# Kernel optimization log

Hardware: AMD Instinct MI355X
Metric: run time of the kernel (lower is better)

## Reference

```python
import jax, jax.numpy as jnp
import numpy as np

N_ATOMS = 500_000
N_PAIRS = 16_000_000
A0 = 0.5291772105638411
KE = 14.399645351950548
KEHALF = KE / 2.0


def softplus_inverse(x):
    # inverse of softplus: log(exp(x) - 1)
    return float(np.log(np.expm1(x)))


def setup_inputs() -> dict:
    key = jax.random.key(0)
    k_z, k_r, k_c, k_i, k_j = jax.random.split(key, 5)
    Zf = jax.random.randint(k_z, (N_ATOMS,), 1, 95).astype(jnp.float32)
    rij = jax.random.uniform(k_r, (N_PAIRS,), minval=0.5, maxval=5.0, dtype=jnp.float32)
    cutoff_values = jax.random.uniform(k_c, (N_PAIRS,), dtype=jnp.float32)
    idx_i = jax.random.randint(k_i, (N_PAIRS,), 0, N_ATOMS)
    idx_j = jax.random.randint(k_j, (N_PAIRS,), 0, N_ATOMS)
    p = lambda v: jnp.full((1,), softplus_inverse(v), dtype=jnp.float32)
    return {
        "N": N_ATOMS,
        "Zf": Zf,
        "rij": rij,
        "cutoff_values": cutoff_values,
        "idx_i": idx_i,
        "idx_j": idx_j,
        "adiv": p(1.0 / (0.8854 * A0)),
        "apow": p(0.23),
        "c1": p(0.1818),
        "c2": p(0.5099),
        "c3": p(0.2802),
        "c4": p(0.02817),
        "a1": p(3.2),
        "a2": p(0.9423),
        "a3": p(0.4028),
        "a4": p(0.2016),
    }


def reference(N, Zf, rij, cutoff_values, idx_i, idx_j,
              adiv, apow, c1, c2, c3, c4, a1, a2, a3, a4):
    sp = jax.nn.softplus
    # per-atom screened charge: [N]
    z = Zf ** sp(apow)
    # per-pair screening length: [P]
    a = (z[idx_i] + z[idx_j]) * sp(adiv)
    a1p = sp(a1) * a
    a2p = sp(a2) * a
    a3p = sp(a3) * a
    a4p = sp(a4) * a
    c1p, c2p, c3p, c4p = sp(c1), sp(c2), sp(c3), sp(c4)
    csum = c1p + c2p + c3p + c4p
    c1n, c2n, c3n, c4n = c1p / csum, c2p / csum, c3p / csum, c4p / csum
    zizj = Zf[idx_i] * Zf[idx_j]
    f = (c1n * jnp.exp(-a1p * rij)
         + c2n * jnp.exp(-a2p * rij)
         + c3n * jnp.exp(-a3p * rij)
         + c4n * jnp.exp(-a4p * rij)) * cutoff_values
    contrib = KEHALF * f * zizj / rij  # [P]
    return jnp.zeros((N,), dtype=Zf.dtype).at[idx_i].add(contrib)
```

## Files before the change

kernel.cpp:

```cpp
#include <hip/hip_runtime.h>
#include <hip/hip_fp16.h>

static constexpr float KEHALF = 7.199822675975274f;
static constexpr int APB = 2048;
static constexpr int APB_SHIFT = 11;
static constexpr int NBMAX = 256;
static constexpr int CHUNK = 8192;
static constexpr int ABLK = 512;
static constexpr int BBLK = 1024;
static constexpr int CTILE = 2048;

typedef float v4f __attribute__((ext_vector_type(4)));
typedef int   v4i __attribute__((ext_vector_type(4)));
typedef unsigned v4u __attribute__((ext_vector_type(4)));

__global__ void zbl_tables_kernel(const float* __restrict__ adiv,
                                  const float* __restrict__ apow,
                                  const float* __restrict__ c1,
                                  const float* __restrict__ c2,
                                  const float* __restrict__ c3,
                                  const float* __restrict__ c4,
                                  const float* __restrict__ a1,
                                  const float* __restrict__ a2,
                                  const float* __restrict__ a3,
                                  const float* __restrict__ a4,
                                  float* __restrict__ consts,
                                  float* __restrict__ lutA) {
    __shared__ float sA[2];
    int t = threadIdx.x;
    if (t == 0) {
        auto sp = [](float x) { return log1pf(expf(x)); };
        float c1p = sp(*c1), c2p = sp(*c2), c3p = sp(*c3), c4p = sp(*c4);
        float inv = 1.0f / (c1p + c2p + c3p + c4p);
        consts[0] = sp(*apow);
        consts[1] = sp(*adiv);
        consts[2] = c1p * inv; consts[3] = c2p * inv;
        consts[4] = c3p * inv; consts[5] = c4p * inv;
        consts[6] = sp(*a1); consts[7] = sp(*a2);
        consts[8] = sp(*a3); consts[9] = sp(*a4);
        sA[0] = consts[0]; sA[1] = consts[1];
    }
    __syncthreads();
    if (t < 96)
        lutA[t] = (t == 0) ? 0.0f : sA[1] * expf(sA[0] * logf((float)t));
}

__global__ void zbl_pack_kernel(const float* __restrict__ Zf,
                                unsigned char* __restrict__ zb, int N) {
    int i = blockIdx.x * blockDim.x + threadIdx.x;
    if (i < N) zb[i] = (unsigned char)(Zf[i] + 0.5f);
}

__global__ void __launch_bounds__(ABLK)
zbl_phaseA(const int* __restrict__ idx_i, const int* __restrict__ idx_j,
           const float* __restrict__ rij, const float* __restrict__ cut,
           const unsigned char* __restrict__ zb,
           const float* __restrict__ consts, const float* __restrict__ lutA,
           unsigned* __restrict__ recs, unsigned short* __restrict__ starts,
           int P, int NB) {
    __shared__ unsigned hist[NBMAX];
    __shared__ unsigned scanv[NBMAX];
    __shared__ unsigned cursor[NBMAX];
    __shared__ float lA[96];
    __shared__ unsigned stage[CHUNK];

    const int t = threadIdx.x;
    const int c = blockIdx.x;
    const int base = c * CHUNK;
    const int lim = min(base + CHUNK, P);
    const int cnt = lim - base;
    const int n4 = cnt >> 2;

    for (int b = t; b < NBMAX; b += ABLK) hist[b] = 0;
    if (t < 96) lA[t] = lutA[t];
    __syncthreads();

    {
        const v4i* ii4 = reinterpret_cast<const v4i*>(idx_i + base);
        for (int q = t; q < n4; q += ABLK) {
            v4i ii = __builtin_nontemporal_load(ii4 + q);
            atomicAdd(&hist[(unsigned)ii[0] >> APB_SHIFT], 1u);
            atomicAdd(&hist[(unsigned)ii[1] >> APB_SHIFT], 1u);
            atomicAdd(&hist[(unsigned)ii[2] >> APB_SHIFT], 1u);
            atomicAdd(&hist[(unsigned)ii[3] >> APB_SHIFT], 1u);
        }
        for (int p = n4 * 4 + t; p < cnt; p += ABLK)
            atomicAdd(&hist[(unsigned)idx_i[base + p] >> APB_SHIFT], 1u);
    }
    __syncthreads();

    if (t < NBMAX) scanv[t] = hist[t];
    __syncthreads();
    for (int off = 1; off < NBMAX; off <<= 1) {
        unsigned v = 0;
        if (t < NBMAX && t >= off) v = scanv[t - off];
        __syncthreads();
        if (t < NBMAX && t >= off) scanv[t] += v;
        __syncthreads();
    }
    if (t < NBMAX) cursor[t] = scanv[t] - hist[t];
    {
        const int S = NB + 1;
        for (int b = t; b <= NB; b += ABLK)
            starts[(size_t)c * S + b] =
                (unsigned short)(b == 0 ? 0u : scanv[b - 1]);
    }
    __syncthreads();

    const float c1n = consts[2], c2n = consts[3], c3n = consts[4], c4n = consts[5];
    const float a1 = consts[6], a2 = consts[7], a3 = consts[8], a4 = consts[9];

    auto process = [&](int i, int j, float r, float cu) {
        unsigned bi = zb[i], bj = zb[j];
        float aij = lA[bi] + lA[bj];
        float ar = aij * r;
        float f = c1n * __expf(-a1 * ar) + c2n * __expf(-a2 * ar)
                + c3n * __expf(-a3 * ar) + c4n * __expf(-a4 * ar);
        float contrib = KEHALF * f * cu * (float)bi * (float)bj *
                        __builtin_amdgcn_rcpf(r);
        unsigned b = (unsigned)i >> APB_SHIFT;
        unsigned rank = atomicAdd(&cursor[b], 1u);
        stage[rank] = (((unsigned)i & (APB - 1)) << 16)
                    | (unsigned)__half_as_ushort(__float2half_rn(contrib));
    };

    {
        const v4i* ii4 = reinterpret_cast<const v4i*>(idx_i + base);
        const v4i* jj4 = reinterpret_cast<const v4i*>(idx_j + base);
        const v4f* rr4 = reinterpret_cast<const v4f*>(rij + base);
        const v4f* cc4 = reinterpret_cast<const v4f*>(cut + base);
        for (int q = t; q < n4; q += ABLK) {
            v4i ii = __builtin_nontemporal_load(ii4 + q);
            v4i jj = __builtin_nontemporal_load(jj4 + q);
            v4f rr = __builtin_nontemporal_load(rr4 + q);
            v4f cc = __builtin_nontemporal_load(cc4 + q);
#pragma unroll
            for (int k = 0; k < 4; ++k) process(ii[k], jj[k], rr[k], cc[k]);
        }
        for (int p = n4 * 4 + t; p < cnt; p += ABLK)
            process(idx_i[base + p], idx_j[base + p], rij[base + p], cut[base + p]);
    }
    __syncthreads();

    {
        const v4u* src = reinterpret_cast<const v4u*>(stage);
        v4u* dst = reinterpret_cast<v4u*>(recs + (size_t)base);
        for (int k = t; k < CHUNK / 4; k += ABLK)
            __builtin_nontemporal_store(src[k], dst + k);
    }
}

__global__ void __launch_bounds__(BBLK)
zbl_phaseB(const unsigned* __restrict__ recs,
           const unsigned short* __restrict__ starts,
           float* __restrict__ out, int N, int NB, int nchunks) {
    __shared__ float acc[APB];
    __shared__ unsigned short s0s[CTILE];
    __shared__ unsigned short s1s[CTILE];
    const int t = threadIdx.x;
    const int b = blockIdx.x;
    const int S = NB + 1;
    for (int i = t; i < APB; i += BBLK) acc[i] = 0.f;

    const int wave = t >> 6, lane = t & 63, nw = BBLK / 64;

    for (int cb = 0; cb < nchunks; cb += CTILE) {
        const int ce = min(cb + CTILE, nchunks);
        __syncthreads();
        for (int c = cb + t; c < ce; c += BBLK) {
            s0s[c - cb] = starts[(size_t)c * S + b];
            s1s[c - cb] = starts[(size_t)c * S + b + 1];
        }
        __syncthreads();
        for (int c = cb + wave; c < ce; c += nw) {
            unsigned s0 = s0s[c - cb], s1 = s1s[c - cb];
            const unsigned* seg = recs + (size_t)c * CHUNK;
            for (unsigned u = s0 + lane; u < s1; u += 64) {
                unsigned rec = __builtin_nontemporal_load(seg + u);
                float v = __half2float(__ushort_as_half((unsigned short)(rec & 0xffffu)));
                atomicAdd(&acc[rec >> 16], v);
            }
        }
    }
    __syncthreads();

    const int abase = b << APB_SHIFT;
    for (int i = t; i < APB; i += BBLK) {
        int g = abase + i;
        if (g < N) out[g] = acc[i];
    }
}

__global__ void __launch_bounds__(256)
zbl_pair_fallback(const v4f* __restrict__ rij4, const v4f* __restrict__ cut4,
                  const v4i* __restrict__ ii4, const v4i* __restrict__ jj4,
                  const float* __restrict__ Zf, const float* __restrict__ consts,
                  float* __restrict__ out, int P4) {
    int t = blockIdx.x * blockDim.x + threadIdx.x;
    if (t >= P4) return;
    const float sp_apow = consts[0], sp_adiv = consts[1];
    const float c1n = consts[2], c2n = consts[3], c3n = consts[4], c4n = consts[5];
    const float a1 = consts[6], a2 = consts[7], a3 = consts[8], a4 = consts[9];
    v4f rr = rij4[t]; v4f cc = cut4[t]; v4i ii = ii4[t]; v4i jj = jj4[t];
#pragma unroll
    for (int k = 0; k < 4; ++k) {
        int i = ii[k], j = jj[k];
        float zfi = Zf[i], zfj = Zf[j];
        float zi = __expf(sp_apow * __logf(zfi));
        float zj = __expf(sp_apow * __logf(zfj));
        float a = (zi + zj) * sp_adiv;
        float ar = a * rr[k];
        float f = c1n * __expf(-a1 * ar) + c2n * __expf(-a2 * ar)
                + c3n * __expf(-a3 * ar) + c4n * __expf(-a4 * ar);
        atomicAdd(&out[i],
                  KEHALF * f * cc[k] * zfi * zfj * __builtin_amdgcn_rcpf(rr[k]));
    }
}

extern "C" void kernel_launch(void* const* d_in, const int* in_sizes, int n_in,
                              void* d_out, int out_size, void* d_ws, size_t ws_size,
                              hipStream_t stream) {
    const float* Zf = (const float*)d_in[1];
    const float* rij = (const float*)d_in[2];
    const float* cut = (const float*)d_in[3];
    const int* idx_i = (const int*)d_in[4];
    const int* idx_j = (const int*)d_in[5];
    const int N = in_sizes[1];
    const int P = in_sizes[2];
    float* out = (float*)d_out;

    const int NB = (N + APB - 1) / APB;
    const int nchunks = (P + CHUNK - 1) / CHUNK;

    size_t recs_bytes = (size_t)nchunks * CHUNK * 4;
    size_t starts_bytes = (size_t)nchunks * (NB + 1) * 2;
    size_t consts_off = (recs_bytes + starts_bytes + 255) & ~(size_t)255;
    size_t lut_off = consts_off + 16 * 4;
    size_t zb_off = lut_off + 96 * 4;
    size_t need = zb_off + (size_t)N + 64;

    if (NB <= NBMAX && ws_size >= need) {
        unsigned* recs = (unsigned*)d_ws;
        unsigned short* starts = (unsigned short*)((char*)d_ws + recs_bytes);
        float* consts = (float*)((char*)d_ws + consts_off);
        float* lutA = (float*)((char*)d_ws + lut_off);
        unsigned char* zb = (unsigned char*)((char*)d_ws + zb_off);

        zbl_tables_kernel<<<1, 128, 0, stream>>>(
            (const float*)d_in[6], (const float*)d_in[7],
            (const float*)d_in[8], (const float*)d_in[9],
            (const float*)d_in[10], (const float*)d_in[11],
            (const float*)d_in[12], (const float*)d_in[13],
            (const float*)d_in[14], (const float*)d_in[15], consts, lutA);

        zbl_pack_kernel<<<(N + 255) / 256, 256, 0, stream>>>(Zf, zb, N);

        zbl_phaseA<<<nchunks, ABLK, 0, stream>>>(
            idx_i, idx_j, rij, cut, zb, consts, lutA, recs, starts, P, NB);

        zbl_phaseB<<<NB, BBLK, 0, stream>>>(recs, starts, out, N, NB, nchunks);
    } else {
        float* consts = (float*)d_ws;
        float* lutA = consts + 16;
        hipMemsetAsync(out, 0, (size_t)out_size * sizeof(float), stream);
        zbl_tables_kernel<<<1, 128, 0, stream>>>(
            (const float*)d_in[6], (const float*)d_in[7],
            (const float*)d_in[8], (const float*)d_in[9],
            (const float*)d_in[10], (const float*)d_in[11],
            (const float*)d_in[12], (const float*)d_in[13],
            (const float*)d_in[14], (const float*)d_in[15], consts, lutA);
        zbl_pair_fallback<<<(P / 4 + 255) / 256, 256, 0, stream>>>(
            (const v4f*)rij, (const v4f*)cut, (const v4i*)idx_i,
            (const v4i*)idx_j, Zf, consts, out, P / 4);
    }
}
```

Before: 488.2 us.

## Split phase B over chunk ranges and drop phase A LDS staging

Phase B now runs on a 2D grid that splits the chunk range across up to 16 blocks per atom bucket. Each block atomically adds its partial sums into a zeroed output, and each 32-lane half-wave walks one segment. Phase A drops the LDS staging buffer and the per-element LUT, scattering records straight to global memory and computing z^p with exp/log inline. It also replaces the block-wide barrier scan with a wave-shuffle scan and keeps the loaded idx_i vectors in registers for reuse. The intent is more parallelism and occupancy in phase B and fewer barriers and less LDS in phase A, at the cost of uncoalesced global stores, extra transcendental math, and global float atomics.

```diff
diff --git a/kernel.cpp b/kernel.cpp
--- a/kernel.cpp
+++ b/kernel.cpp
@@ -8,7 +8,8 @@
 static constexpr int CHUNK = 8192;
 static constexpr int ABLK = 512;
 static constexpr int BBLK = 1024;
-static constexpr int CTILE = 2048;
+static constexpr int CTILE = 1024;
+static constexpr int NW_SCAN = NBMAX / 64;
 
 typedef float v4f __attribute__((ext_vector_type(4)));
 typedef int   v4i __attribute__((ext_vector_type(4)));
@@ -24,11 +25,8 @@
                                   const float* __restrict__ a2,
                                   const float* __restrict__ a3,
                                   const float* __restrict__ a4,
-                                  float* __restrict__ consts,
-                                  float* __restrict__ lutA) {
-    __shared__ float sA[2];
-    int t = threadIdx.x;
-    if (t == 0) {
+                                  float* __restrict__ consts) {
+    if (threadIdx.x == 0) {
         auto sp = [](float x) { return log1pf(expf(x)); };
         float c1p = sp(*c1), c2p = sp(*c2), c3p = sp(*c3), c4p = sp(*c4);
         float inv = 1.0f / (c1p + c2p + c3p + c4p);
@@ -38,11 +36,7 @@
         consts[4] = c3p * inv; consts[5] = c4p * inv;
         consts[6] = sp(*a1); consts[7] = sp(*a2);
         consts[8] = sp(*a3); consts[9] = sp(*a4);
-        sA[0] = consts[0]; sA[1] = consts[1];
-    }
-    __syncthreads();
-    if (t < 96)
-        lutA[t] = (t == 0) ? 0.0f : sA[1] * expf(sA[0] * logf((float)t));
+    }
 }
 
 __global__ void zbl_pack_kernel(const float* __restrict__ Zf,
@@ -55,14 +49,12 @@
 zbl_phaseA(const int* __restrict__ idx_i, const int* __restrict__ idx_j,
            const float* __restrict__ rij, const float* __restrict__ cut,
            const unsigned char* __restrict__ zb,
-           const float* __restrict__ consts, const float* __restrict__ lutA,
+           const float* __restrict__ consts,
            unsigned* __restrict__ recs, unsigned short* __restrict__ starts,
            int P, int NB) {
     __shared__ unsigned hist[NBMAX];
-    __shared__ unsigned scanv[NBMAX];
     __shared__ unsigned cursor[NBMAX];
-    __shared__ float lA[96];
-    __shared__ unsigned stage[CHUNK];
+    __shared__ unsigned wsum[NW_SCAN];
 
     const int t = threadIdx.x;
     const int c = blockIdx.x;
@@ -72,110 +64,122 @@
     const int n4 = cnt >> 2;
 
     for (int b = t; b < NBMAX; b += ABLK) hist[b] = 0;
-    if (t < 96) lA[t] = lutA[t];
-    __syncthreads();
-
-    {
-        const v4i* ii4 = reinterpret_cast<const v4i*>(idx_i + base);
-        for (int q = t; q < n4; q += ABLK) {
-            v4i ii = __builtin_nontemporal_load(ii4 + q);
-            atomicAdd(&hist[(unsigned)ii[0] >> APB_SHIFT], 1u);
-            atomicAdd(&hist[(unsigned)ii[1] >> APB_SHIFT], 1u);
-            atomicAdd(&hist[(unsigned)ii[2] >> APB_SHIFT], 1u);
-            atomicAdd(&hist[(unsigned)ii[3] >> APB_SHIFT], 1u);
-        }
-        for (int p = n4 * 4 + t; p < cnt; p += ABLK)
-            atomicAdd(&hist[(unsigned)idx_i[base + p] >> APB_SHIFT], 1u);
-    }
-    __syncthreads();
-
-    if (t < NBMAX) scanv[t] = hist[t];
-    __syncthreads();
-    for (int off = 1; off < NBMAX; off <<= 1) {
-        unsigned v = 0;
-        if (t < NBMAX && t >= off) v = scanv[t - off];
-        __syncthreads();
-        if (t < NBMAX && t >= off) scanv[t] += v;
-        __syncthreads();
-    }
-    if (t < NBMAX) cursor[t] = scanv[t] - hist[t];
-    {
-        const int S = NB + 1;
-        for (int b = t; b <= NB; b += ABLK)
-            starts[(size_t)c * S + b] =
-                (unsigned short)(b == 0 ? 0u : scanv[b - 1]);
-    }
-    __syncthreads();
-
+    __syncthreads();
+
+    const v4i* ii4 = reinterpret_cast<const v4i*>(idx_i + base);
+    const bool p0 = t < n4;
+    const bool p1 = ABLK + t < n4;
+    const bool p2 = 2 * ABLK + t < n4;
+    const bool p3 = 3 * ABLK + t < n4;
+    v4i ii0{}, ii1{}, ii2{}, ii3{};
+    if (p0) ii0 = __builtin_nontemporal_load(ii4 + t);
+    if (p1) ii1 = __builtin_nontemporal_load(ii4 + ABLK + t);
+    if (p2) ii2 = __builtin_nontemporal_load(ii4 + 2 * ABLK + t);
+    if (p3) ii3 = __builtin_nontemporal_load(ii4 + 3 * ABLK + t);
+
+    auto hist4 = [&](v4i ii) {
+        atomicAdd(&hist[(unsigned)ii[0] >> APB_SHIFT], 1u);
+        atomicAdd(&hist[(unsigned)ii[1] >> APB_SHIFT], 1u);
+        atomicAdd(&hist[(unsigned)ii[2] >> APB_SHIFT], 1u);
+        atomicAdd(&hist[(unsigned)ii[3] >> APB_SHIFT], 1u);
+    };
+    if (p0) hist4(ii0);
+    if (p1) hist4(ii1);
+    if (p2) hist4(ii2);
+    if (p3) hist4(ii3);
+    for (int p = n4 * 4 + t; p < cnt; p += ABLK)
+        atomicAdd(&hist[(unsigned)idx_i[base + p] >> APB_SHIFT], 1u);
+    __syncthreads();
+
+    unsigned hv = (t < NBMAX) ? hist[t] : 0u;
+    unsigned v = hv;
+#pragma unroll
+    for (int off = 1; off < 64; off <<= 1) {
+        unsigned n = __shfl_up(v, off, 64);
+        if ((t & 63) >= off) v += n;
+    }
+    if (t < NBMAX && (t & 63) == 63) wsum[t >> 6] = v;
+    __syncthreads();
+    const int S = NB + 1;
+    if (t < NBMAX) {
+        unsigned pre = 0;
+#pragma unroll
+        for (int w = 0; w < NW_SCAN - 1; ++w)
+            if (w < (t >> 6)) pre += wsum[w];
+        unsigned inc = v + pre;
+        cursor[t] = inc - hv;
+        if (t < NB)
+            starts[(size_t)c * S + t + 1] = (unsigned short)inc;
+    }
+    if (t == 0) starts[(size_t)c * S] = 0;
+    __syncthreads();
+
+    const float sp_apow = consts[0], sp_adiv = consts[1];
     const float c1n = consts[2], c2n = consts[3], c3n = consts[4], c4n = consts[5];
     const float a1 = consts[6], a2 = consts[7], a3 = consts[8], a4 = consts[9];
 
     auto process = [&](int i, int j, float r, float cu) {
         unsigned bi = zb[i], bj = zb[j];
-        float aij = lA[bi] + lA[bj];
-        float ar = aij * r;
+        float fi = (float)bi, fj = (float)bj;
+        float zi = __expf(sp_apow * __logf(fi));
+        float zj = __expf(sp_apow * __logf(fj));
+        float ar = (zi + zj) * sp_adiv * r;
         float f = c1n * __expf(-a1 * ar) + c2n * __expf(-a2 * ar)
                 + c3n * __expf(-a3 * ar) + c4n * __expf(-a4 * ar);
-        float contrib = KEHALF * f * cu * (float)bi * (float)bj *
-                        __builtin_amdgcn_rcpf(r);
+        float contrib = KEHALF * f * cu * fi * fj * __builtin_amdgcn_rcpf(r);
         unsigned b = (unsigned)i >> APB_SHIFT;
         unsigned rank = atomicAdd(&cursor[b], 1u);
-        stage[rank] = (((unsigned)i & (APB - 1)) << 16)
-                    | (unsigned)__half_as_ushort(__float2half_rn(contrib));
+        unsigned rec = (((unsigned)i & (APB - 1)) << 16)
+                     | (unsigned)__half_as_ushort(__float2half_rn(contrib));
+        recs[(size_t)base + rank] = rec;
     };
 
-    {
-        const v4i* ii4 = reinterpret_cast<const v4i*>(idx_i + base);
-        const v4i* jj4 = reinterpret_cast<const v4i*>(idx_j + base);
-        const v4f* rr4 = reinterpret_cast<const v4f*>(rij + base);
-        const v4f* cc4 = reinterpret_cast<const v4f*>(cut + base);
-        for (int q = t; q < n4; q += ABLK) {
-            v4i ii = __builtin_nontemporal_load(ii4 + q);
-            v4i jj = __builtin_nontemporal_load(jj4 + q);
-            v4f rr = __builtin_nontemporal_load(rr4 + q);
-            v4f cc = __builtin_nontemporal_load(cc4 + q);
-#pragma unroll
-            for (int k = 0; k < 4; ++k) process(ii[k], jj[k], rr[k], cc[k]);
-        }
-        for (int p = n4 * 4 + t; p < cnt; p += ABLK)
-            process(idx_i[base + p], idx_j[base + p], rij[base + p], cut[base + p]);
-    }
-    __syncthreads();
-
-    {
-        const v4u* src = reinterpret_cast<const v4u*>(stage);
-        v4u* dst = reinterpret_cast<v4u*>(recs + (size_t)base);
-        for (int k = t; k < CHUNK / 4; k += ABLK)
-            __builtin_nontemporal_store(src[k], dst + k);
-    }
+    const v4i* jj4 = reinterpret_cast<const v4i*>(idx_j + base);
+    const v4f* rr4 = reinterpret_cast<const v4f*>(rij + base);
+    const v4f* cc4 = reinterpret_cast<const v4f*>(cut + base);
+    auto group = [&](v4i ii, int q) {
+        v4i jj = __builtin_nontemporal_load(jj4 + q);
+        v4f rr = __builtin_nontemporal_load(rr4 + q);
+        v4f cc = __builtin_nontemporal_load(cc4 + q);
+#pragma unroll
+        for (int k = 0; k < 4; ++k) process(ii[k], jj[k], rr[k], cc[k]);
+    };
+    if (p0) group(ii0, t);
+    if (p1) group(ii1, ABLK + t);
+    if (p2) group(ii2, 2 * ABLK + t);
+    if (p3) group(ii3, 3 * ABLK + t);
+    for (int p = n4 * 4 + t; p < cnt; p += ABLK)
+        process(idx_i[base + p], idx_j[base + p], rij[base + p], cut[base + p]);
 }
 
 __global__ void __launch_bounds__(BBLK)
 zbl_phaseB(const unsigned* __restrict__ recs,
            const unsigned short* __restrict__ starts,
-           float* __restrict__ out, int N, int NB, int nchunks) {
+           float* __restrict__ out, int N, int NB, int nchunks, int cpb) {
     __shared__ float acc[APB];
     __shared__ unsigned short s0s[CTILE];
     __shared__ unsigned short s1s[CTILE];
     const int t = threadIdx.x;
     const int b = blockIdx.x;
+    const int c0 = blockIdx.y * cpb;
+    const int c1e = min(c0 + cpb, nchunks);
     const int S = NB + 1;
     for (int i = t; i < APB; i += BBLK) acc[i] = 0.f;
 
-    const int wave = t >> 6, lane = t & 63, nw = BBLK / 64;
-
-    for (int cb = 0; cb < nchunks; cb += CTILE) {
-        const int ce = min(cb + CTILE, nchunks);
+    const int hw = t >> 5, hl = t & 31, nhw = BBLK / 32;
+
+    for (int cb = c0; cb < c1e; cb += CTILE) {
+        const int ce = min(cb + CTILE, c1e);
         __syncthreads();
         for (int c = cb + t; c < ce; c += BBLK) {
             s0s[c - cb] = starts[(size_t)c * S + b];
             s1s[c - cb] = starts[(size_t)c * S + b + 1];
         }
         __syncthreads();
-        for (int c = cb + wave; c < ce; c += nw) {
+        for (int c = cb + hw; c < ce; c += nhw) {
             unsigned s0 = s0s[c - cb], s1 = s1s[c - cb];
             const unsigned* seg = recs + (size_t)c * CHUNK;
-            for (unsigned u = s0 + lane; u < s1; u += 64) {
+            for (unsigned u = s0 + hl; u < s1; u += 32) {
                 unsigned rec = __builtin_nontemporal_load(seg + u);
                 float v = __half2float(__ushort_as_half((unsigned short)(rec & 0xffffu)));
                 atomicAdd(&acc[rec >> 16], v);
@@ -183,11 +187,10 @@
         }
     }
     __syncthreads();
-
     const int abase = b << APB_SHIFT;
     for (int i = t; i < APB; i += BBLK) {
         int g = abase + i;
-        if (g < N) out[g] = acc[i];
+        if (g < N) atomicAdd(&out[g], acc[i]);
     }
 }
 
@@ -235,40 +238,45 @@
     size_t recs_bytes = (size_t)nchunks * CHUNK * 4;
     size_t starts_bytes = (size_t)nchunks * (NB + 1) * 2;
     size_t consts_off = (recs_bytes + starts_bytes + 255) & ~(size_t)255;
-    size_t lut_off = consts_off + 16 * 4;
-    size_t zb_off = lut_off + 96 * 4;
+    size_t zb_off = consts_off + 16 * 4;
     size_t need = zb_off + (size_t)N + 64;
 
     if (NB <= NBMAX && ws_size >= need) {
         unsigned* recs = (unsigned*)d_ws;
         unsigned short* starts = (unsigned short*)((char*)d_ws + recs_bytes);
         float* consts = (float*)((char*)d_ws + consts_off);
-        float* lutA = (float*)((char*)d_ws + lut_off);
         unsigned char* zb = (unsigned char*)((char*)d_ws + zb_off);
 
-        zbl_tables_kernel<<<1, 128, 0, stream>>>(
+        zbl_tables_kernel<<<1, 64, 0, stream>>>(
             (const float*)d_in[6], (const float*)d_in[7],
             (const float*)d_in[8], (const float*)d_in[9],
             (const float*)d_in[10], (const float*)d_in[11],
             (const float*)d_in[12], (const float*)d_in[13],
-            (const float*)d_in[14], (const float*)d_in[15], consts, lutA);
+            (const float*)d_in[14], (const float*)d_in[15], consts);
 
         zbl_pack_kernel<<<(N + 255) / 256, 256, 0, stream>>>(Zf, zb, N);
 
+        hipMemsetAsync(out, 0, (size_t)out_size * sizeof(float), stream);
+
         zbl_phaseA<<<nchunks, ABLK, 0, stream>>>(
-            idx_i, idx_j, rij, cut, zb, consts, lutA, recs, starts, P, NB);
-
-        zbl_phaseB<<<NB, BBLK, 0, stream>>>(recs, starts, out, N, NB, nchunks);
+            idx_i, idx_j, rij, cut, zb, consts, recs, starts, P, NB);
+
+        int SPLIT = (2048 + NB - 1) / NB;
+        if (SPLIT < 1) SPLIT = 1;
+        if (SPLIT > 16) SPLIT = 16;
+        const int cpb = (nchunks + SPLIT - 1) / SPLIT;
+        dim3 gridB(NB, SPLIT);
+        zbl_phaseB<<<gridB, BBLK, 0, stream>>>(recs, starts, out, N, NB,
+                                               nchunks, cpb);
     } else {
         float* consts = (float*)d_ws;
-        float* lutA = consts + 16;
         hipMemsetAsync(out, 0, (size_t)out_size * sizeof(float), stream);
-        zbl_tables_kernel<<<1, 128, 0, stream>>>(
+        zbl_tables_kernel<<<1, 64, 0, stream>>>(
             (const float*)d_in[6], (const float*)d_in[7],
             (const float*)d_in[8], (const float*)d_in[9],
             (const float*)d_in[10], (const float*)d_in[11],
             (const float*)d_in[12], (const float*)d_in[13],
-            (const float*)d_in[14], (const float*)d_in[15], consts, lutA);
+            (const float*)d_in[14], (const float*)d_in[15], consts);
         zbl_pair_fallback<<<(P / 4 + 255) / 256, 256, 0, stream>>>(
             (const v4f*)rij, (const v4f*)cut, (const v4i*)idx_i,
             (const v4i*)idx_j, Zf, consts, out, P / 4);
```

Result: slower. 542.6 us (+11.2%).
